# Performance work log

Measured on AMD Instinct MI355X. Metric: run time of the kernel, lower is better.

Reference implementation:

```python
import jax, jax.numpy as jnp
import numpy as np
from jax import lax

BLOCK = 32
THRESH = 0.1
EPS = 1e-5
_BN_SCALE = 1.0 / float(np.sqrt(1.0 + EPS))  # eval BatchNorm with default stats (mean=0, var=1)


def _conv3d(x, w):
    return lax.conv_general_dilated(x, w, (1, 1, 1), 'VALID',
                                    dimension_numbers=('NCDHW', 'OIDHW', 'NCDHW'))


def _convT3d(x, w):
    # torch ConvTranspose3d(k=4, s=2, p=0): s -> 2s+2
    return lax.conv_transpose(x, w, (2, 2, 2), 'VALID',
                              dimension_numbers=('NCDHW', 'IODHW', 'NCDHW'))


def _bn(x):
    return x * _BN_SCALE


def _maxpool(x, k):
    return lax.reduce_window(x, -jnp.inf, lax.max, (1, 1, k, k, k), (1, 1, k, k, k), 'VALID')


def _basic_block(x, w1, w2, upsample):
    if upsample:
        h = _convT3d(x, w1)                                   # s -> 2s+2
    else:
        h = jnp.pad(x, ((0, 0), (0, 0), (2, 2), (2, 2), (2, 2)), mode='edge')  # ReplicationPad3d(2)
        h = _conv3d(h, w1)                                    # s+4 -> s+2
    h = jax.nn.relu(_bn(h))
    return _bn(_conv3d(h, w2))                                # -> 2s (upsample) or s


def _pred_block(x, wa, wb, w_lin, b_lin):
    h = jax.nn.relu(_bn(_conv3d(x, wa)))   # 32 -> 30
    h = _maxpool(h, 3)                     # -> 10
    h = jax.nn.relu(_bn(_conv3d(h, wb)))   # -> 8
    h = _maxpool(h, 4)                     # -> 2
    h = h.reshape(h.shape[0], -1)          # [N, (C//4)*8] = [N, 64]
    return jax.nn.softmax(h @ w_lin.T + b_lin, axis=1)


def _forward(tsdf, prev, w_up_t, w_up_c, w_ts1, w_ts2, w_b1a, w_b1b, w_pa, w_pb, w_lin, b_lin):
    G = tsdf.shape[-1] // BLOCK
    # carve the dense tsdf into [G^3, 1, BLOCK, BLOCK, BLOCK] blocks in (x,y,z) row-major key order
    t = tsdf[0, 0].reshape(G, BLOCK, G, BLOCK, G, BLOCK)
    t = t.transpose(0, 2, 4, 1, 3, 5).reshape(G * G * G, 1, BLOCK, BLOCK, BLOCK)
    prevs = _basic_block(prev, w_up_t, w_up_c, True)           # [N, 32, 32,32,32]
    tfeat = _basic_block(t, w_ts1, w_ts2, False)               # [N, 16, 32,32,32]
    feat = _basic_block(jnp.concatenate([prevs, tfeat], axis=1), w_b1a, w_b1b, False)  # [N, 32, 32^3]
    pred = _pred_block(feat, w_pa, w_pb, w_lin, b_lin)         # [N, 3]
    return pred


def setup_inputs():
    key = jax.random.key(0)
    ks = jax.random.split(key, 12)
    s = 0.05
    return {
        'tsdf': jax.random.normal(ks[0], (1, 1, 96, 96, 96), jnp.float32),
        'prev': jax.random.normal(ks[1], (27, 32, 16, 16, 16), jnp.float32),
        'w_up_t': jax.random.normal(ks[2], (32, 32, 4, 4, 4), jnp.float32) * s,
        'w_up_c': jax.random.normal(ks[3], (32, 32, 3, 3, 3), jnp.float32) * s,
        'w_ts1': jax.random.normal(ks[4], (16, 1, 3, 3, 3), jnp.float32) * s,
        'w_ts2': jax.random.normal(ks[5], (16, 16, 3, 3, 3), jnp.float32) * s,
        'w_b1a': jax.random.normal(ks[6], (32, 48, 3, 3, 3), jnp.float32) * s,
        'w_b1b': jax.random.normal(ks[7], (32, 32, 3, 3, 3), jnp.float32) * s,
        'w_pa': jax.random.normal(ks[8], (16, 32, 3, 3, 3), jnp.float32) * s,
        'w_pb': jax.random.normal(ks[9], (8, 16, 3, 3, 3), jnp.float32) * s,
        'w_lin': jax.random.normal(ks[10], (3, 64), jnp.float32) * s,
        'b_lin': jnp.zeros((3,), jnp.float32),
    }


def reference(tsdf, prev, w_up_t, w_up_c, w_ts1, w_ts2, w_b1a, w_b1b, w_pa, w_pb, w_lin, b_lin):
    pred = _forward(tsdf, prev, w_up_t, w_up_c, w_ts1, w_ts2,
                    w_b1a, w_b1b, w_pa, w_pb, w_lin, b_lin)
    # eval-mode threshold gating: which blocks would be split and recursively refined
    mixed = pred[:, -1] > THRESH
    return pred, mixed
```

## Files before the change

### kernel.cpp

```cpp
#include <hip/hip_runtime.h>
#include <math.h>

#define BNS 0.9999950000374997f

static inline int cdiv(int a, int b) { return (a + b - 1) / b; }

typedef short short8 __attribute__((ext_vector_type(8)));
typedef float f32x4 __attribute__((ext_vector_type(4)));
typedef unsigned int u32x4 __attribute__((ext_vector_type(4)));

__device__ __forceinline__ unsigned short f2bf(float f) {
    unsigned int u = __float_as_uint(f);
    u += 0x7fffu + ((u >> 16) & 1u);
    return (unsigned short)(u >> 16);
}
__device__ __forceinline__ float bf2f(unsigned short u) {
    return __uint_as_float(((unsigned int)u) << 16);
}

__device__ __forceinline__ int xcd_swz(int bid, int nwg) {
    int q = nwg >> 3, r = nwg & 7;
    int xcd = bid & 7;
    int idx = bid >> 3;
    return (xcd < r ? xcd * (q + 1) : r * (q + 1) + (xcd - r) * q) + idx;
}

#define U1 ((size_t)39304 * 48)
#define U2 ((size_t)46656 * 48)
#define U3 ((size_t)39304 * 32)

__global__ void k_tr_conv(const float* __restrict__ w, float* __restrict__ wT,
                          int CIN, int COUT) {
    int i = blockIdx.x * 256 + threadIdx.x;
    int total = CIN * COUT * 27;
    if (i >= total) return;
    int co = i % COUT;
    int tap = (i / COUT) % 27;
    int ci = i / (COUT * 27);
    wT[i] = w[(co * CIN + ci) * 27 + tap];
}

__global__ void k_trw(const float* __restrict__ w, unsigned short* __restrict__ Bt,
                      int CIN, int CHUNKS, int NCO) {
    int i = blockIdx.x * 256 + threadIdx.x;
    int total = CHUNKS * 27 * NCO * 32;
    if (i >= total) return;
    int cil = i & 31;
    int n = (i >> 5) % NCO;
    int t = (i / (32 * NCO)) % 27;
    int c = i / (32 * NCO * 27);
    int ci = c * 32 + cil;
    float v = (ci < CIN) ? w[(n * CIN + ci) * 27 + t] : 0.f;
    Bt[i] = f2bf(v);
}

__global__ void k_trwT(const float* __restrict__ w, unsigned short* __restrict__ Bt) {
    int i = blockIdx.x * 256 + threadIdx.x;
    if (i >= 64 * 32 * 32) return;
    int cil = i & 31;
    int co = (i >> 5) & 31;
    int tap = i >> 10;
    Bt[i] = f2bf(w[(cil * 32 + co) * 64 + tap]);
}

__global__ __launch_bounds__(256) void k_tprev(const float* __restrict__ prev,
                                               unsigned short* __restrict__ out) {
    __shared__ float t32[32][65];
    int n = blockIdx.y;
    int p0 = blockIdx.x * 64;
    int tid = threadIdx.x;
    #pragma unroll
    for (int it = 0; it < 8; ++it) {
        int idx = it * 256 + tid;
        int ci = idx >> 6;
        int dp = idx & 63;
        t32[ci][dp] = prev[((size_t)n * 32 + ci) * 4096 + p0 + dp];
    }
    __syncthreads();
    int dp = tid >> 2;
    int cq = (tid & 3) * 8;
    u32x4 u;
    #pragma unroll
    for (int j = 0; j < 4; ++j) {
        u[j] = (unsigned int)f2bf(t32[cq + 2 * j][dp]) |
               ((unsigned int)f2bf(t32[cq + 2 * j + 1][dp]) << 16);
    }
    *(u32x4*)(out + ((size_t)n * 4096 + p0 + dp) * 32 + cq) = u;
}

__global__ __launch_bounds__(256) void k_ts1(const float* __restrict__ tsdf,
                                             const float* __restrict__ wT,
                                             unsigned short* __restrict__ buf1, int nbase) {
    int n = blockIdx.y;
    int ng = nbase + n;
    int a1 = ng / 9, b1 = (ng / 3) % 3, c1 = ng % 3;
    int s = blockIdx.x * 256 + threadIdx.x;
    if (s >= 39304) return;
    int z = s / (34 * 34);
    int r = s % (34 * 34);
    int y = r / 34;
    int x = r % 34;

    int base = (a1 * 32 * 96 + b1 * 32) * 96 + c1 * 32;
    int offs[27];
    #pragma unroll
    for (int kz = 0; kz < 3; ++kz) {
        int zz = z + kz - 2; zz = zz < 0 ? 0 : (zz > 31 ? 31 : zz);
        #pragma unroll
        for (int ky = 0; ky < 3; ++ky) {
            int yy = y + ky - 2; yy = yy < 0 ? 0 : (yy > 31 ? 31 : yy);
            #pragma unroll
            for (int kx = 0; kx < 3; ++kx) {
                int xx = x + kx - 2; xx = xx < 0 ? 0 : (xx > 31 ? 31 : xx);
                offs[(kz * 3 + ky) * 3 + kx] = zz * 9216 + yy * 96 + xx;
            }
        }
    }

    float acc[16];
    #pragma unroll
    for (int c = 0; c < 16; ++c) acc[c] = 0.f;

    const float* p = tsdf + base;
    #pragma unroll
    for (int t = 0; t < 27; ++t) {
        float v = p[offs[t]];
        const float* wp = wT + t * 16;
        #pragma unroll
        for (int co = 0; co < 16; ++co) acc[co] = fmaf(v, wp[co], acc[co]);
    }

    unsigned short* o = buf1 + (size_t)n * U1 + (size_t)s * 48 + 32;
    #pragma unroll
    for (int co = 0; co < 16; ++co) {
        float v = acc[co] * BNS;
        o[co] = f2bf(v > 0.f ? v : 0.f);
    }
}

template <int CSTRIDE, int CINOFF, int KRLOC, int CH, int NCO, int OCST, int OCOFF,
          int IND, int OUTD, int OD2, int OPAD, bool RELU>
__global__ __launch_bounds__(256) void
k_cl(const unsigned short* __restrict__ in, const unsigned short* __restrict__ Bt,
     unsigned short* __restrict__ out, size_t inNS, size_t outNS) {
    constexpr int TZ = 2, TY = 4;
    constexpr int XE = OUTD + 2;
    constexpr int XG = (OUTD + 15) / 16;
    constexpr int NSUB = (TZ * TY * XG) / 4;
    constexpr int NT = NCO / 16;
    constexpr int ZT = (OUTD + TZ - 1) / TZ;
    constexpr int YT = (OUTD + TY - 1) / TY;
    constexpr int POS = (TZ + 2) * (TY + 2) * XE;
    constexpr int ITER = (POS * 4 + 255) / 256;

    __shared__ __align__(16) unsigned char smem[POS * 64];

    int wg = xcd_swz(blockIdx.x, gridDim.x);
    int n = wg / (ZT * YT);
    int r0 = wg - n * (ZT * YT);
    int zt = r0 / YT, yt = r0 - zt * YT;
    int z0 = zt * TZ, y0 = yt * TY;

    int tid = threadIdx.x;
    int lane = tid & 63;
    int q = lane & 15, g = lane >> 4;
    int wv = tid >> 6;

    const unsigned char* inN = (const unsigned char*)(in + (size_t)n * inNS);

    int posj[NSUB];
    #pragma unroll
    for (int j = 0; j < NSUB; ++j) {
        int s = wv * NSUB + j;
        int sz = s / (TY * XG);
        int rm = s - sz * (TY * XG);
        int sy = rm / XG;
        int sxg = rm - sy * XG;
        int x = sxg * 16 + q;
        x = x < OUTD ? x : OUTD - 1;
        posj[j] = (sz * (TY + 2) + sy) * XE + x;
    }

    f32x4 acc[NSUB][NT];
    #pragma unroll
    for (int j = 0; j < NSUB; ++j)
        #pragma unroll
        for (int nt = 0; nt < NT; ++nt)
            #pragma unroll
            for (int rr = 0; rr < 4; ++rr) acc[j][nt][rr] = 0.f;

    for (int c = 0; c < CH; ++c) {
        if (c) __syncthreads();
        short8 tmp[ITER];
        #pragma unroll
        for (int it = 0; it < ITER; ++it) {
            int i = it * 256 + tid;
            short8 v = {0, 0, 0, 0, 0, 0, 0, 0};
            if (i < POS * 4) {
                int slot = i & 3;
                int pos = i >> 2;
                if (c * 32 + slot * 8 < KRLOC) {
                    int dx = pos % XE;
                    int rm = pos / XE;
                    int dy = rm % (TY + 2);
                    int dz = rm / (TY + 2);
                    int iz = z0 + dz; iz = iz < IND - 1 ? iz : IND - 1;
                    int iy = y0 + dy; iy = iy < IND - 1 ? iy : IND - 1;
                    v = *(const short8*)(inN +
                        ((size_t)(iz * IND + iy) * IND + dx) * (CSTRIDE * 2) +
                        CINOFF * 2 + c * 64 + slot * 16);
                }
            }
            tmp[it] = v;
        }
        #pragma unroll
        for (int it = 0; it < ITER; ++it) {
            int i = it * 256 + tid;
            if (i < POS * 4) *(short8*)(smem + (size_t)i * 16) = tmp[it];
        }
        __syncthreads();

        const unsigned short* bc = Bt + (size_t)(c * 27) * NCO * 32 + (size_t)q * 32 + g * 8;
        #pragma unroll
        for (int t = 0; t < 27; ++t) {
            const int kz = t / 9, ky = (t / 3) % 3, kx = t % 3;
            const int toff = ((kz * (TY + 2) + ky) * XE + kx) * 64 + g * 16;
            short8 bq[NT];
            #pragma unroll
            for (int nt = 0; nt < NT; ++nt)
                bq[nt] = *(const short8*)(bc + ((size_t)t * NCO + nt * 16) * 32);
            #pragma unroll
            for (int j = 0; j < NSUB; ++j) {
                short8 a = *(const short8*)(smem + posj[j] * 64 + toff);
                #pragma unroll
                for (int nt = 0; nt < NT; ++nt)
                    acc[j][nt] = __builtin_amdgcn_mfma_f32_16x16x32_bf16(a, bq[nt], acc[j][nt], 0, 0, 0);
            }
        }
    }

    unsigned short* outN = out + (size_t)n * outNS;
    #pragma unroll
    for (int j = 0; j < NSUB; ++j) {
        int s = wv * NSUB + j;
        int sz = s / (TY * XG);
        int rm = s - sz * (TY * XG);
        int sy = rm / XG;
        int sxg = rm - sy * XG;
        int z = z0 + sz, y = y0 + sy;
        if (z < OUTD && y < OUTD) {
            #pragma unroll
            for (int rr = 0; rr < 4; ++rr) {
                int x = sxg * 16 + g * 4 + rr;
                if (x < OUTD) {
                    size_t ob = ((size_t)((z + OPAD) * OD2 + y + OPAD) * OD2 + (x + OPAD)) * OCST + OCOFF;
                    #pragma unroll
                    for (int nt = 0; nt < NT; ++nt) {
                        float v = acc[j][nt][rr] * BNS;
                        if (RELU) v = v > 0.f ? v : 0.f;
                        outN[ob + nt * 16 + q] = f2bf(v);
                    }
                }
            }
        }
    }
}

__global__ __launch_bounds__(256) void k_pad(unsigned short* __restrict__ buf2, int ncnt) {
    int i = blockIdx.x * 256 + threadIdx.x;
    int total = ncnt * 46656 * 6;
    if (i >= total) return;
    int slot = i % 6;
    int pos = (i / 6) % 46656;
    int nl = i / (6 * 46656);
    int x = pos % 36, y = (pos / 36) % 36, z = pos / 1296;
    if (x >= 2 && x < 34 && y >= 2 && y < 34 && z >= 2 && z < 34) return;
    int sx = x < 2 ? 2 : (x > 33 ? 33 : x);
    int sy = y < 2 ? 2 : (y > 33 ? 33 : y);
    int sz = z < 2 ? 2 : (z > 33 ? 33 : z);
    int src = (sz * 36 + sy) * 36 + sx;
    unsigned short* bn = buf2 + (size_t)nl * U2;
    *(u32x4*)(bn + (size_t)pos * 48 + slot * 8) =
        *(const u32x4*)(bn + (size_t)src * 48 + slot * 8);
}

__global__ __launch_bounds__(192) void
k_cT(const unsigned short* __restrict__ prevT, const unsigned short* __restrict__ Bt,
     unsigned short* __restrict__ buf1, int nbase) {
    constexpr int XE = 19, YS = 5, S = 2 * YS * XE;
    constexpr int MT = 68;

    __shared__ __align__(16) unsigned char smem[S * 80];

    int n = blockIdx.z;
    int ng = nbase + n;
    int q = blockIdx.y;
    int px = q & 1, py = (q >> 1) & 1, pz = q >> 2;
    int bt = blockIdx.x;
    int yt = bt % 5, z = bt / 5;
    int ty0 = yt * 4;

    int tid = threadIdx.x;
    int lane = tid & 63;
    int g = lane >> 4;
    int wv = tid >> 6;

    int mb = wv * 32 + (lane & 15);
    int m0 = mb < MT ? mb : MT - 1;
    int m1 = (mb + 16) < MT ? (mb + 16) : MT - 1;
    int dy0 = m0 / 17, x0 = m0 - dy0 * 17;
    int dy1 = m1 / 17, x1 = m1 - dy1 * 17;
    int pb0 = (dy0 * XE + x0) * 80 + g * 16;
    int pb1 = (dy1 * XE + x1) * 80 + g * 16;

    const unsigned short* inN = prevT + (size_t)ng * 4096 * 32;

    for (int i = tid; i < S * 4; i += 192) {
        int pos = i >> 2, slot = i & 3;
        int dz = pos / (YS * XE);
        int rem = pos - dz * (YS * XE);
        int dyy = rem / XE;
        int ix = rem - dyy * XE;
        int iz = z - 1 + dz;
        int iy = ty0 - 1 + dyy;
        int ixx = ix - 1;
        u32x4 v = {0u, 0u, 0u, 0u};
        if ((unsigned)iz < 16u && (unsigned)iy < 16u && (unsigned)ixx < 16u) {
            v = *(const u32x4*)(inN + ((size_t)(iz * 16 + iy) * 16 + ixx) * 32 + slot * 8);
        }
        *(u32x4*)(smem + pos * 80 + slot * 16) = v;
    }
    __syncthreads();

    int kz0 = 1 - pz, ky0 = 1 - py, kx0 = 1 - px;

    f32x4 acc[2][2];
    #pragma unroll
    for (int s2 = 0; s2 < 2; ++s2)
        #pragma unroll
        for (int nt = 0; nt < 2; ++nt)
            #pragma unroll
            for (int rr = 0; rr < 4; ++rr) acc[s2][nt][rr] = 0.f;

    #pragma unroll
    for (int cz = 0; cz < 2; ++cz)
        #pragma unroll
        for (int cy = 0; cy < 2; ++cy)
            #pragma unroll
            for (int cx = 0; cx < 2; ++cx) {
                int toff = ((cz * YS + cy) * XE + cx) * 80;
                int tapg = (((kz0 + 2 * cz) * 4 + (ky0 + 2 * cy)) * 4 + (kx0 + 2 * cx));
                const unsigned short* bb =
                    Bt + ((size_t)tapg * 32 + (lane & 15)) * 32 + g * 8;
                short8 a0 = *(const short8*)(smem + pb0 + toff);
                short8 a1 = *(const short8*)(smem + pb1 + toff);
                #pragma unroll
                for (int nt = 0; nt < 2; ++nt) {
                    short8 bf = *(const short8*)(bb + (size_t)nt * 16 * 32);
                    acc[0][nt] = __builtin_amdgcn_mfma_f32_16x16x32_bf16(a0, bf, acc[0][nt], 0, 0, 0);
                    acc[1][nt] = __builtin_amdgcn_mfma_f32_16x16x32_bf16(a1, bf, acc[1][nt], 0, 0, 0);
                }
            }

    unsigned short* outN = buf1 + (size_t)n * U1;
    int co0 = lane & 15;
    #pragma unroll
    for (int sub = 0; sub < 2; ++sub) {
        #pragma unroll
        for (int rr = 0; rr < 4; ++rr) {
            int m = wv * 32 + sub * 16 + g * 4 + rr;
            if (m < MT) {
                int dy = m / 17, tx = m - dy * 17;
                if (ty0 + dy < 17) {
                    int oz = 2 * z + pz, oy = 2 * (ty0 + dy) + py, ox = 2 * tx + px;
                    size_t ob = ((size_t)(oz * 34 + oy) * 34 + ox) * 48;
                    #pragma unroll
                    for (int nt = 0; nt < 2; ++nt) {
                        float v = acc[sub][nt][rr] * BNS;
                        outN[ob + nt * 16 + co0] = f2bf(v > 0.f ? v : 0.f);
                    }
                }
            }
        }
    }
}

__global__ __launch_bounds__(256) void k_pool3(const unsigned short* __restrict__ pa,
                                               float* __restrict__ out,
                                               int nbase, int ncnt) {
    int i = blockIdx.x * 256 + threadIdx.x;
    if (i >= ncnt * 16000) return;
    int c = i & 15;
    int rest = i >> 4;
    int x = rest % 10;
    int y = (rest / 10) % 10;
    int z = (rest / 100) % 10;
    int nl = rest / 1000;
    const unsigned short* p = pa + (size_t)nl * U2;
    float m = -INFINITY;
    #pragma unroll
    for (int dz = 0; dz < 3; ++dz)
        #pragma unroll
        for (int dy = 0; dy < 3; ++dy)
            #pragma unroll
            for (int dx = 0; dx < 3; ++dx)
                m = fmaxf(m, bf2f(p[((size_t)((3 * z + dz) * 30 + 3 * y + dy) * 30 +
                                    (3 * x + dx)) * 16 + c]));
    out[((size_t)(nbase + nl) * 16 + c) * 1000 + (z * 100 + y * 10 + x)] = m;
}

template <int CIN, int COUT, int IND, int OUTD>
__global__ __launch_bounds__(256) void k_conv3(const float* __restrict__ in,
                                               const float* __restrict__ wT,
                                               float* __restrict__ out) {
    constexpr int IN3 = IND * IND * IND;
    constexpr int OD3 = OUTD * OUTD * OUTD;
    int n = blockIdx.y;
    int s = blockIdx.x * 256 + threadIdx.x;
    if (s >= OD3) return;
    int z = s / (OUTD * OUTD);
    int r = s % (OUTD * OUTD);
    int y = r / OUTD;
    int x = r % OUTD;

    int offs[27];
    #pragma unroll
    for (int kz = 0; kz < 3; ++kz)
        #pragma unroll
        for (int ky = 0; ky < 3; ++ky)
            #pragma unroll
            for (int kx = 0; kx < 3; ++kx)
                offs[(kz * 3 + ky) * 3 + kx] = ((z + kz) * IND + y + ky) * IND + x + kx;

    float acc[COUT];
    #pragma unroll
    for (int c = 0; c < COUT; ++c) acc[c] = 0.f;

    const float* inN = in + (size_t)n * CIN * IN3;
    for (int ci = 0; ci < CIN; ++ci) {
        const float* pc = inN + (size_t)ci * IN3;
        const float* wci = wT + ci * 27 * COUT;
        #pragma unroll
        for (int t = 0; t < 27; ++t) {
            float v = pc[offs[t]];
            const float* wp = wci + t * COUT;
            #pragma unroll
            for (int co = 0; co < COUT; ++co) acc[co] = fmaf(v, wp[co], acc[co]);
        }
    }

    float* o = out + (size_t)n * COUT * OD3 + s;
    #pragma unroll
    for (int co = 0; co < COUT; ++co) {
        float v = acc[co] * BNS;
        o[(size_t)co * OD3] = v > 0.f ? v : 0.f;
    }
}

__global__ __launch_bounds__(64) void k_final(const float* __restrict__ p2,
                                              const float* __restrict__ wlin,
                                              const float* __restrict__ blin,
                                              float* __restrict__ dout) {
    int n = blockIdx.x;
    int t = threadIdx.x;
    int c = t >> 3, dz = (t >> 2) & 1, dy = (t >> 1) & 1, dx = t & 1;
    const float* p = p2 + ((size_t)n * 8 + c) * 512;
    float m = -INFINITY;
    #pragma unroll
    for (int iz = 0; iz < 4; ++iz)
        #pragma unroll
        for (int iy = 0; iy < 4; ++iy)
            #pragma unroll
            for (int ix = 0; ix < 4; ++ix)
                m = fmaxf(m, p[((dz * 4 + iz) * 8 + dy * 4 + iy) * 8 + dx * 4 + ix]);
    __shared__ float h[64];
    __shared__ float lg[3];
    h[t] = m;
    __syncthreads();
    if (t < 3) {
        float acc = blin[t];
        for (int k = 0; k < 64; ++k) acc += h[k] * wlin[t * 64 + k];
        lg[t] = acc;
    }
    __syncthreads();
    if (t == 0) {
        float mx = fmaxf(fmaxf(lg[0], lg[1]), lg[2]);
        float e0 = expf(lg[0] - mx), e1 = expf(lg[1] - mx), e2 = expf(lg[2] - mx);
        float inv = 1.f / (e0 + e1 + e2);
        dout[n * 3 + 0] = e0 * inv;
        dout[n * 3 + 1] = e1 * inv;
        dout[n * 3 + 2] = e2 * inv;
        dout[81 + n] = (e2 * inv) > 0.1f ? 1.0f : 0.0f;
    }
}

extern "C" void kernel_launch(void* const* d_in, const int* in_sizes, int n_in,
                              void* d_out, int out_size, void* d_ws, size_t ws_size,
                              hipStream_t stream) {
    const float* tsdf  = (const float*)d_in[0];
    const float* prev  = (const float*)d_in[1];
    const float* w_upt = (const float*)d_in[2];
    const float* w_upc = (const float*)d_in[3];
    const float* w_ts1 = (const float*)d_in[4];
    const float* w_ts2 = (const float*)d_in[5];
    const float* w_b1a = (const float*)d_in[6];
    const float* w_b1b = (const float*)d_in[7];
    const float* w_pa  = (const float*)d_in[8];
    const float* w_pb  = (const float*)d_in[9];
    const float* w_lin = (const float*)d_in[10];
    const float* b_lin = (const float*)d_in[11];
    float* dout = (float*)d_out;

    char* base = (char*)d_ws;
    size_t off = 0;
    auto alB = [&](size_t bytes) {
        off = (off + 255) & ~(size_t)255;
        void* p = base + off;
        off += bytes;
        return p;
    };

    float* P1      = (float*)alB((size_t)27 * 16 * 1000 * 4);
    float* P2      = (float*)alB((size_t)27 * 8 * 512 * 4);
    float* wT_ts1  = (float*)alB(27 * 16 * 4);
    float* wT_pb   = (float*)alB((size_t)16 * 27 * 8 * 4);
    unsigned short* prevT   = (unsigned short*)alB((size_t)27 * 4096 * 32 * 2);
    unsigned short* BtT_upt = (unsigned short*)alB((size_t)64 * 32 * 32 * 2);
    unsigned short* Bt_upc  = (unsigned short*)alB((size_t)27 * 32 * 32 * 2);
    unsigned short* Bt_ts2  = (unsigned short*)alB((size_t)27 * 16 * 32 * 2);
    unsigned short* Bt_b1a  = (unsigned short*)alB((size_t)2 * 27 * 32 * 32 * 2);
    unsigned short* Bt_b1b  = (unsigned short*)alB((size_t)27 * 32 * 32 * 2);
    unsigned short* Bt_pa   = (unsigned short*)alB((size_t)27 * 16 * 32 * 2);

    size_t fixed = (off + 255) & ~(size_t)255;
    size_t per_block = (U1 + U2 + U3) * 2 + 768;
    size_t avail = ws_size > fixed ? ws_size - fixed : 0;
    int NB = (int)(avail / per_block);
    if (NB > 27) NB = 27;
    if (NB < 1) NB = 1;

    unsigned short* buf1 = (unsigned short*)alB((size_t)NB * U1 * 2);
    unsigned short* buf2 = (unsigned short*)alB((size_t)NB * U2 * 2);
    unsigned short* buf3 = (unsigned short*)alB((size_t)NB * U3 * 2);

    k_tr_conv<<<cdiv(1 * 16 * 27, 256), 256, 0, stream>>>(w_ts1, wT_ts1, 1, 16);
    k_tr_conv<<<cdiv(16 * 8 * 27, 256), 256, 0, stream>>>(w_pb, wT_pb, 16, 8);
    k_trwT<<<cdiv(64 * 32 * 32, 256), 256, 0, stream>>>(w_upt, BtT_upt);
    k_trw<<<cdiv(1 * 27 * 32 * 32, 256), 256, 0, stream>>>(w_upc, Bt_upc, 32, 1, 32);
    k_trw<<<cdiv(1 * 27 * 16 * 32, 256), 256, 0, stream>>>(w_ts2, Bt_ts2, 16, 1, 16);
    k_trw<<<cdiv(2 * 27 * 32 * 32, 256), 256, 0, stream>>>(w_b1a, Bt_b1a, 48, 2, 32);
    k_trw<<<cdiv(1 * 27 * 32 * 32, 256), 256, 0, stream>>>(w_b1b, Bt_b1b, 32, 1, 32);
    k_trw<<<cdiv(1 * 27 * 16 * 32, 256), 256, 0, stream>>>(w_pa, Bt_pa, 32, 1, 16);
    k_tprev<<<dim3(64, 27), 256, 0, stream>>>(prev, prevT);

    for (int n0 = 0; n0 < 27; n0 += NB) {
        int nc = 27 - n0 < NB ? 27 - n0 : NB;

        k_cT<<<dim3(17 * 5, 8, nc), 192, 0, stream>>>(prevT, BtT_upt, buf1, n0);
        k_ts1<<<dim3(cdiv(39304, 256), nc), 256, 0, stream>>>(tsdf, wT_ts1, buf1, n0);

        k_cl<48, 0, 32, 1, 32, 48, 0, 34, 32, 36, 2, false>
            <<<nc * 16 * 8, 256, 0, stream>>>(buf1, Bt_upc, buf2, U1, U2);
        k_cl<48, 32, 16, 1, 16, 48, 32, 34, 32, 36, 2, false>
            <<<nc * 16 * 8, 256, 0, stream>>>(buf1, Bt_ts2, buf2, U1, U2);

        k_pad<<<cdiv(nc * 46656 * 6, 256), 256, 0, stream>>>(buf2, nc);

        k_cl<48, 0, 48, 2, 32, 32, 0, 36, 34, 34, 0, true>
            <<<nc * 17 * 9, 256, 0, stream>>>(buf2, Bt_b1a, buf3, U2, U3);

        k_cl<32, 0, 32, 1, 32, 32, 0, 34, 32, 32, 0, false>
            <<<nc * 16 * 8, 256, 0, stream>>>(buf3, Bt_b1b, buf1, U3, U1);

        k_cl<32, 0, 32, 1, 16, 16, 0, 32, 30, 30, 0, true>
            <<<nc * 15 * 8, 256, 0, stream>>>(buf1, Bt_pa, buf2, U1, U2);

        k_pool3<<<cdiv(nc * 16000, 256), 256, 0, stream>>>(buf2, P1, n0, nc);
    }

    k_conv3<16, 8, 10, 8><<<dim3(cdiv(512, 256), 27), 256, 0, stream>>>(P1, wT_pb, P2);
    k_final<<<27, 64, 0, stream>>>(P2, w_lin, b_lin, dout);
}
```

Baseline: 616.8 us.

## Reuse LDS A-fragments across ky taps by mapping each wave to a y-column

Each wave now owns one z-slice and one 16-wide x group and handles all TY rows. For each (kz,kx) it loads TY+2 A fragments from shared memory once and reuses them across the three ky taps, instead of reloading an A fragment for every tap and sub-tile. This cuts LDS read traffic per MFMA. For the b1a conv (34-wide output, 3 x-groups) the block grows to 384 threads so every x group gets a wave. The cost is more accumulator and fragment registers per thread, which may lower occupancy.

```diff
diff --git a/kernel.cpp b/kernel.cpp
--- a/kernel.cpp
+++ b/kernel.cpp
@@ -139,19 +139,18 @@
 }
 
 template <int CSTRIDE, int CINOFF, int KRLOC, int CH, int NCO, int OCST, int OCOFF,
-          int IND, int OUTD, int OD2, int OPAD, bool RELU>
-__global__ __launch_bounds__(256) void
-k_cl(const unsigned short* __restrict__ in, const unsigned short* __restrict__ Bt,
+          int IND, int OUTD, int OD2, int OPAD, bool RELU, int XG>
+__global__ __launch_bounds__(XG * 128) void
+k_cy(const unsigned short* __restrict__ in, const unsigned short* __restrict__ Bt,
      unsigned short* __restrict__ out, size_t inNS, size_t outNS) {
     constexpr int TZ = 2, TY = 4;
     constexpr int XE = OUTD + 2;
-    constexpr int XG = (OUTD + 15) / 16;
-    constexpr int NSUB = (TZ * TY * XG) / 4;
     constexpr int NT = NCO / 16;
     constexpr int ZT = (OUTD + TZ - 1) / TZ;
     constexpr int YT = (OUTD + TY - 1) / TY;
     constexpr int POS = (TZ + 2) * (TY + 2) * XE;
-    constexpr int ITER = (POS * 4 + 255) / 256;
+    constexpr int NTH = XG * 128;
+    constexpr int ITER = (POS * 4 + NTH - 1) / NTH;
 
     __shared__ __align__(16) unsigned char smem[POS * 64];
 
@@ -165,36 +164,28 @@
     int lane = tid & 63;
     int q = lane & 15, g = lane >> 4;
     int wv = tid >> 6;
+    int sz = wv / XG, sxg = wv - sz * XG;
 
     const unsigned char* inN = (const unsigned char*)(in + (size_t)n * inNS);
 
-    int posj[NSUB];
-    #pragma unroll
-    for (int j = 0; j < NSUB; ++j) {
-        int s = wv * NSUB + j;
-        int sz = s / (TY * XG);
-        int rm = s - sz * (TY * XG);
-        int sy = rm / XG;
-        int sxg = rm - sy * XG;
-        int x = sxg * 16 + q;
-        x = x < OUTD ? x : OUTD - 1;
-        posj[j] = (sz * (TY + 2) + sy) * XE + x;
-    }
-
-    f32x4 acc[NSUB][NT];
-    #pragma unroll
-    for (int j = 0; j < NSUB; ++j)
+    int x = sxg * 16 + q;
+    x = x < OUTD ? x : OUTD - 1;
+    int wbase = (sz * (TY + 2) * XE + x) * 64 + g * 16;
+
+    f32x4 acc[TY][NT];
+    #pragma unroll
+    for (int sy = 0; sy < TY; ++sy)
         #pragma unroll
         for (int nt = 0; nt < NT; ++nt)
             #pragma unroll
-            for (int rr = 0; rr < 4; ++rr) acc[j][nt][rr] = 0.f;
+            for (int rr = 0; rr < 4; ++rr) acc[sy][nt][rr] = 0.f;
 
     for (int c = 0; c < CH; ++c) {
         if (c) __syncthreads();
         short8 tmp[ITER];
         #pragma unroll
         for (int it = 0; it < ITER; ++it) {
-            int i = it * 256 + tid;
+            int i = it * NTH + tid;
             short8 v = {0, 0, 0, 0, 0, 0, 0, 0};
             if (i < POS * 4) {
                 int slot = i & 3;
@@ -215,48 +206,53 @@
         }
         #pragma unroll
         for (int it = 0; it < ITER; ++it) {
-            int i = it * 256 + tid;
+            int i = it * NTH + tid;
             if (i < POS * 4) *(short8*)(smem + (size_t)i * 16) = tmp[it];
         }
         __syncthreads();
 
         const unsigned short* bc = Bt + (size_t)(c * 27) * NCO * 32 + (size_t)q * 32 + g * 8;
         #pragma unroll
-        for (int t = 0; t < 27; ++t) {
-            const int kz = t / 9, ky = (t / 3) % 3, kx = t % 3;
-            const int toff = ((kz * (TY + 2) + ky) * XE + kx) * 64 + g * 16;
-            short8 bq[NT];
-            #pragma unroll
-            for (int nt = 0; nt < NT; ++nt)
-                bq[nt] = *(const short8*)(bc + ((size_t)t * NCO + nt * 16) * 32);
-            #pragma unroll
-            for (int j = 0; j < NSUB; ++j) {
-                short8 a = *(const short8*)(smem + posj[j] * 64 + toff);
+        for (int kz = 0; kz < 3; ++kz) {
+            #pragma unroll
+            for (int kx = 0; kx < 3; ++kx) {
+                short8 a[TY + 2];
                 #pragma unroll
-                for (int nt = 0; nt < NT; ++nt)
-                    acc[j][nt] = __builtin_amdgcn_mfma_f32_16x16x32_bf16(a, bq[nt], acc[j][nt], 0, 0, 0);
+                for (int yy = 0; yy < TY + 2; ++yy)
+                    a[yy] = *(const short8*)(smem + wbase +
+                              ((kz * (TY + 2) + yy) * XE + kx) * 64);
+                #pragma unroll
+                for (int ky = 0; ky < 3; ++ky) {
+                    const int t = (kz * 3 + ky) * 3 + kx;
+                    short8 bq[NT];
+                    #pragma unroll
+                    for (int nt = 0; nt < NT; ++nt)
+                        bq[nt] = *(const short8*)(bc + ((size_t)t * NCO + nt * 16) * 32);
+                    #pragma unroll
+                    for (int sy = 0; sy < TY; ++sy)
+                        #pragma unroll
+                        for (int nt = 0; nt < NT; ++nt)
+                            acc[sy][nt] = __builtin_amdgcn_mfma_f32_16x16x32_bf16(
+                                a[sy + ky], bq[nt], acc[sy][nt], 0, 0, 0);
+                }
             }
         }
     }
 
     unsigned short* outN = out + (size_t)n * outNS;
-    #pragma unroll
-    for (int j = 0; j < NSUB; ++j) {
-        int s = wv * NSUB + j;
-        int sz = s / (TY * XG);
-        int rm = s - sz * (TY * XG);
-        int sy = rm / XG;
-        int sxg = rm - sy * XG;
-        int z = z0 + sz, y = y0 + sy;
+    int z = z0 + sz;
+    #pragma unroll
+    for (int sy = 0; sy < TY; ++sy) {
+        int y = y0 + sy;
         if (z < OUTD && y < OUTD) {
             #pragma unroll
             for (int rr = 0; rr < 4; ++rr) {
-                int x = sxg * 16 + g * 4 + rr;
-                if (x < OUTD) {
-                    size_t ob = ((size_t)((z + OPAD) * OD2 + y + OPAD) * OD2 + (x + OPAD)) * OCST + OCOFF;
+                int xo = sxg * 16 + g * 4 + rr;
+                if (xo < OUTD) {
+                    size_t ob = ((size_t)((z + OPAD) * OD2 + y + OPAD) * OD2 + (xo + OPAD)) * OCST + OCOFF;
                     #pragma unroll
                     for (int nt = 0; nt < NT; ++nt) {
-                        float v = acc[j][nt][rr] * BNS;
+                        float v = acc[sy][nt][rr] * BNS;
                         if (RELU) v = v > 0.f ? v : 0.f;
                         outN[ob + nt * 16 + q] = f2bf(v);
                     }
@@ -559,20 +555,20 @@
         k_cT<<<dim3(17 * 5, 8, nc), 192, 0, stream>>>(prevT, BtT_upt, buf1, n0);
         k_ts1<<<dim3(cdiv(39304, 256), nc), 256, 0, stream>>>(tsdf, wT_ts1, buf1, n0);
 
-        k_cl<48, 0, 32, 1, 32, 48, 0, 34, 32, 36, 2, false>
+        k_cy<48, 0, 32, 1, 32, 48, 0, 34, 32, 36, 2, false, 2>
             <<<nc * 16 * 8, 256, 0, stream>>>(buf1, Bt_upc, buf2, U1, U2);
-        k_cl<48, 32, 16, 1, 16, 48, 32, 34, 32, 36, 2, false>
+        k_cy<48, 32, 16, 1, 16, 48, 32, 34, 32, 36, 2, false, 2>
             <<<nc * 16 * 8, 256, 0, stream>>>(buf1, Bt_ts2, buf2, U1, U2);
 
         k_pad<<<cdiv(nc * 46656 * 6, 256), 256, 0, stream>>>(buf2, nc);
 
-        k_cl<48, 0, 48, 2, 32, 32, 0, 36, 34, 34, 0, true>
-            <<<nc * 17 * 9, 256, 0, stream>>>(buf2, Bt_b1a, buf3, U2, U3);
-
-        k_cl<32, 0, 32, 1, 32, 32, 0, 34, 32, 32, 0, false>
+        k_cy<48, 0, 48, 2, 32, 32, 0, 36, 34, 34, 0, true, 3>
+            <<<nc * 17 * 9, 384, 0, stream>>>(buf2, Bt_b1a, buf3, U2, U3);
+
+        k_cy<32, 0, 32, 1, 32, 32, 0, 34, 32, 32, 0, false, 2>
             <<<nc * 16 * 8, 256, 0, stream>>>(buf3, Bt_b1b, buf1, U3, U1);
 
-        k_cl<32, 0, 32, 1, 16, 16, 0, 32, 30, 30, 0, true>
+        k_cy<32, 0, 32, 1, 16, 16, 0, 32, 30, 30, 0, true, 2>
             <<<nc * 15 * 8, 256, 0, stream>>>(buf1, Bt_pa, buf2, U1, U2);
 
         k_pool3<<<cdiv(nc * 16000, 256), 256, 0, stream>>>(buf2, P1, n0, nc);
```

Result: slower. 657.4 us (+6.6%).
